# Optimization experiments

Measured on AMD Instinct MI355X. Metric: run time of the kernel, lower is better.

The kernel has to match this reference:

```python
import jax, jax.numpy as jnp
import numpy as np

B, N, K1, M, D = 8, 4096, 17, 2, 256
NT = B * N          # total nodes
EPS = 1e-5          # PyG LayerNorm default eps


def setup_inputs() -> dict:
    key = jax.random.key(0)
    ks = jax.random.split(key, 13)
    s = 1.0 / np.sqrt(D)
    return {
        "x": jax.random.normal(ks[0], (NT, M, D), jnp.float32),
        "knn_edges": jax.random.randint(ks[1], (B, N, K1), 0, N),
        "edge_mask": jax.random.bernoulli(ks[2], 0.9, (B, N, K1)),
        "W0": jax.random.normal(ks[3], (D, D), jnp.float32) * s,
        "b0": jnp.zeros((D,), jnp.float32),
        "g0": jnp.ones((D,), jnp.float32),
        "be0": jnp.zeros((D,), jnp.float32),
        "a0": jnp.full((1,), 0.25, jnp.float32),
        "W1": jax.random.normal(ks[4], (D, D), jnp.float32) * s,
        "b1": jnp.zeros((D,), jnp.float32),
        "g1": jnp.ones((D,), jnp.float32),
        "be1": jnp.zeros((D,), jnp.float32),
        "a1": jnp.full((1,), 0.25, jnp.float32),
    }


def knn_to_edges(knn_edges, edge_mask):
    # drop self column 0, add per-graph batch offsets; keep fixed E with 0/1 weights
    e = knn_edges[:, :, 1:]                       # [B, N, K]
    m = edge_mask[:, :, 1:]
    off = (jnp.arange(B) * N)[:, None, None]      # [B,1,1]
    src = jnp.broadcast_to(jnp.arange(N)[None, :, None] + off, e.shape).reshape(-1)
    dst = (e + off).reshape(-1)
    w = m.reshape(-1).astype(jnp.float32)         # invalid edges -> weight 0
    return src, dst, w


def gcn_conv(h_in, W, b, src, dst, w):
    # PyG GCNConv: add self-loops (weight 1), symmetric normalization
    h = h_in @ W                                            # [NT, D]
    deg = jax.ops.segment_sum(w, dst, num_segments=NT) + 1.0
    dinv = jax.lax.rsqrt(deg)                               # [NT]
    norm = dinv[src] * w * dinv[dst]                        # [E]
    agg = jax.ops.segment_sum(norm[:, None] * h[src], dst, num_segments=NT)
    agg = agg + (dinv * dinv)[:, None] * h                  # self-loop term
    return agg + b


def graph_layernorm(x, g, b):
    # PyG LayerNorm mode='graph', batch=None: normalize over all nodes+features
    xc = x - jnp.mean(x)
    std = jnp.sqrt(jnp.mean(xc * xc))
    return g * (xc / (std + EPS)) + b


def prelu(x, a):
    return jnp.where(x >= 0, x, a * x)


def reference(x, knn_edges, edge_mask, W0, b0, g0, be0, a0, W1, b1, g1, be1, a1):
    src, dst, w = knn_to_edges(knn_edges, edge_mask)
    h = x[:, 0, :]                                          # [NT, D]
    for (W, b, g, be, a) in ((W0, b0, g0, be0, a0), (W1, b1, g1, be1, a1)):
        h = gcn_conv(h, W, b, src, dst, w)
        h = graph_layernorm(h, g, be)
        h = prelu(h, a)
    return h
```

## Files before the change

### kernel.cpp

```cpp
#include <hip/hip_runtime.h>
#include <hip/hip_bf16.h>
#include <stdint.h>

#define B_   8
#define N_   4096
#define K1_  17
#define D_   256
#define NT_  (B_*N_)
#define E16_ (NT_*16)
#define NP_  (NT_*D_)
#define EPS_ 1e-5f

typedef __attribute__((ext_vector_type(8))) short short8v;
typedef __attribute__((ext_vector_type(4))) float f32x4;

__device__ __forceinline__ unsigned short f2bfu(float f){
  unsigned u = __float_as_uint(f);
  unsigned r = (u + 0x7FFFu + ((u>>16)&1u)) >> 16;
  return (unsigned short)r;
}
__device__ __forceinline__ short f2bf(float f){ return (short)f2bfu(f); }
__device__ __forceinline__ unsigned pkbf(float lo, float hi){
  return (unsigned)f2bfu(lo) | ((unsigned)f2bfu(hi) << 16);
}
__device__ __forceinline__ float bf2f(short s){
  return __uint_as_float(((unsigned)(unsigned short)s) << 16);
}
__device__ __forceinline__ void unpack2(unsigned u, float& lo, float& hi){
  lo = __uint_as_float(u << 16);
  hi = __uint_as_float(u & 0xFFFF0000u);
}

__global__ __launch_bounds__(256) void k_prep(const float* __restrict__ W0,
                                              const float* __restrict__ W1,
                                              short* __restrict__ Wt0,
                                              short* __restrict__ Wt1,
                                              int* __restrict__ degcnt,
                                              const unsigned int* __restrict__ mw,
                                              int* __restrict__ flag){
  if (blockIdx.x < 128){
    const float* W  = (blockIdx.x & 1) ? W1  : W0;
    short*       Wt = (blockIdx.x & 1) ? Wt1 : Wt0;
    int tile = blockIdx.x >> 1;
    int ti = tile >> 3, tj = tile & 7;
    __shared__ float sm[32][33];
    int r = threadIdx.x >> 5, c = threadIdx.x & 31;
    #pragma unroll
    for (int i=0;i<4;i++)
      sm[r + i*8][c] = W[(ti*32 + r + i*8)*256 + tj*32 + c];
    __syncthreads();
    #pragma unroll
    for (int i=0;i<4;i++){
      int rr = r + i*8;
      Wt[(size_t)(tj*32 + rr)*256 + ti*32 + c] = f2bf(sm[c][rr]);
    }
  } else {
    int ib = blockIdx.x - 128;
    int i  = ib*256 + threadIdx.x;
    degcnt[i] = 0;
    if (ib == 0){
      __shared__ int s_int, s_f32;
      if (threadIdx.x==0){ s_int=1; s_f32=1; }
      __syncthreads();
      int bad_i=0, bad_f=0;
      #pragma unroll
      for (int j=0;j<4;j++){
        unsigned w = mw[threadIdx.x*4 + j];
        if (!(w==0u || w==1u))          bad_i=1;
        if (!(w==0u || w==0x3F800000u)) bad_f=1;
      }
      if (bad_i) atomicAnd(&s_int, 0);
      if (bad_f) atomicAnd(&s_f32, 0);
      __syncthreads();
      if (threadIdx.x==0) *flag = s_int ? 0 : (s_f32 ? 1 : 2);
    }
  }
}

__device__ __forceinline__ bool mask_at(const void* maskp, int f, int idx){
  if (f==0) return ((const int*)maskp)[idx] != 0;
  if (f==1) return ((const float*)maskp)[idx] != 0.0f;
  return ((const unsigned char*)maskp)[idx] != 0;
}

__global__ void k_deg(const int* __restrict__ knn, const void* __restrict__ maskp,
                      const int* __restrict__ flag, int* __restrict__ degcnt){
  int f = *flag;
  int bid = blockIdx.x;
  int e = ((bid & 7) << 16) + ((bid >> 3) << 8) + threadIdx.x;
  int node = e >> 4;
  int k    = (e & 15) + 1;
  int idx  = node*K1_ + k;
  if (mask_at(maskp, f, idx)){
    int b   = node >> 12;
    int dst = knn[idx] + (b<<12);
    atomicAdd(&degcnt[dst], 1);
  }
}

__global__ void k_scan(const int* __restrict__ degcnt, int* __restrict__ rowptr,
                       int* __restrict__ fillptr, float* __restrict__ dinv){
  __shared__ int wsum[16];
  int t = threadIdx.x;
  int lane = t & 63, wid = t >> 6;
  int base = t*32;
  int loc[32]; int tot = 0;
  #pragma unroll
  for (int i=0;i<32;i++){ loc[i] = degcnt[base+i]; tot += loc[i]; }
  int inc = tot;
  #pragma unroll
  for (int off=1; off<64; off<<=1){
    int v = __shfl_up(inc, off, 64);
    if (lane >= off) inc += v;
  }
  if (lane == 63) wsum[wid] = inc;
  __syncthreads();
  int woff = 0;
  #pragma unroll
  for (int i=0;i<16;i++) if (i < wid) woff += wsum[i];
  int run = woff + inc - tot;
  #pragma unroll
  for (int i=0;i<32;i++){
    int v = base+i;
    rowptr[v]  = run;
    fillptr[v] = run;
    dinv[v]    = rsqrtf((float)loc[i] + 1.0f);
    run += loc[i];
  }
  if (t==1023) rowptr[NT_] = run;
}

__device__ __forceinline__ void g_mfma4(const short* lA, const short* lB,
                                        int wr, int wc, int lr, int qg,
                                        f32x4 (&acc)[4][4]){
  #pragma unroll
  for (int ks=0; ks<2; ks++){
    short8v af[4], bfr[4];
    #pragma unroll
    for (int m=0;m<4;m++){
      int row = wr*64 + m*16 + lr;
      af[m] = *(const short8v*)(lA + (row*8 + ((ks*4+qg) ^ (row&7)))*8);
    }
    #pragma unroll
    for (int n=0;n<4;n++){
      int coln = wc*64 + n*16 + lr;
      bfr[n] = *(const short8v*)(lB + (coln*8 + ((ks*4+qg) ^ (coln&7)))*8);
    }
    #pragma unroll
    for (int m=0;m<4;m++)
      #pragma unroll
      for (int n=0;n<4;n++)
        acc[m][n] = __builtin_amdgcn_mfma_f32_16x16x32_bf16(af[m], bfr[n], acc[m][n], 0, 0, 0);
  }
}

__device__ __forceinline__ void g_cstore(short* __restrict__ C, int rowB,
                                         int wr, int wc, int lr, int qg,
                                         const f32x4 (&acc)[4][4]){
  #pragma unroll
  for (int m=0;m<4;m++){
    int crow = rowB + wr*64 + m*16 + qg*4;
    #pragma unroll
    for (int n=0;n<4;n++){
      int ccol = wc*64 + n*16 + lr;
      #pragma unroll
      for (int r=0;r<4;r++)
        C[(size_t)(crow + r)*256 + ccol] = f2bf(acc[m][n][r]);
    }
  }
}

__global__ __launch_bounds__(512, 4) void k_gemm_x_fill(const float* __restrict__ X,
                                                        const short* __restrict__ Wt,
                                                        short* __restrict__ C,
                                                        const int* __restrict__ knn,
                                                        const void* __restrict__ maskp,
                                                        const int* __restrict__ flag,
                                                        int* __restrict__ fillptr,
                                                        int* __restrict__ col){
  __shared__ short lA[128*64];
  __shared__ short lB[256*64];
  if (blockIdx.x >= 256){
    int f = *flag;
    int fb = (int)blockIdx.x - 256;
    int e  = ((fb & 7) << 16) + ((fb >> 3) << 9) + threadIdx.x;
    int node = e >> 4;
    int k    = (e & 15) + 1;
    int idx  = node*K1_ + k;
    if (mask_at(maskp, f, idx)){
      int b   = node >> 12;
      int dst = knn[idx] + (b<<12);
      int pos = atomicAdd(&fillptr[dst], 1);
      col[pos] = node;
    }
    return;
  }
  int lb   = (int)(blockIdx.x & 7)*32 + (int)(blockIdx.x >> 3);
  int rowB = lb*128;

  int t    = threadIdx.x;
  int wave = t >> 6, lane = t & 63;
  int lr   = lane & 15, qg = lane >> 4;
  int wr   = wave >> 2, wc = wave & 3;

  f32x4 acc[4][4];
  #pragma unroll
  for (int m=0;m<4;m++)
    #pragma unroll
    for (int n=0;n<4;n++) acc[m][n] = (f32x4){0.f,0.f,0.f,0.f};

  int saA[2], scA[2], saB[4], scB[4];
  #pragma unroll
  for (int i=0;i<2;i++){ int e = t + i*512; saA[i] = e>>3; scA[i] = e&7; }
  #pragma unroll
  for (int i=0;i<4;i++){ int e = t + i*512; saB[i] = e>>3; scB[i] = e&7; }

  float4 rax[2], ray[2]; uint4 rb[4];
  #pragma unroll
  for (int i=0;i<2;i++){
    const float* ap = X + (size_t)(rowB+saA[i])*512 + scA[i]*8;
    rax[i] = *(const float4*)ap;
    ray[i] = *(const float4*)(ap+4);
  }
  #pragma unroll
  for (int i=0;i<4;i++)
    rb[i] = *(const uint4*)(Wt + (size_t)saB[i]*256 + scB[i]*8);

  for (int kc=0; kc<4; kc++){
    if (kc) __syncthreads();
    #pragma unroll
    for (int i=0;i<2;i++){
      int ph = saA[i]*8 + (scA[i] ^ (saA[i]&7));
      uint4 cv;
      cv.x = pkbf(rax[i].x, rax[i].y); cv.y = pkbf(rax[i].z, rax[i].w);
      cv.z = pkbf(ray[i].x, ray[i].y); cv.w = pkbf(ray[i].z, ray[i].w);
      *(uint4*)(lA + ph*8) = cv;
    }
    #pragma unroll
    for (int i=0;i<4;i++){
      int ph = saB[i]*8 + (scB[i] ^ (saB[i]&7));
      *(uint4*)(lB + ph*8) = rb[i];
    }
    __syncthreads();
    if (kc < 3){
      #pragma unroll
      for (int i=0;i<2;i++){
        const float* ap = X + (size_t)(rowB+saA[i])*512 + (kc+1)*64 + scA[i]*8;
        rax[i] = *(const float4*)ap;
        ray[i] = *(const float4*)(ap+4);
      }
      #pragma unroll
      for (int i=0;i<4;i++)
        rb[i] = *(const uint4*)(Wt + (size_t)saB[i]*256 + (kc+1)*64 + scB[i]*8);
    }
    g_mfma4(lA, lB, wr, wc, lr, qg, acc);
  }
  g_cstore(C, rowB, wr, wc, lr, qg, acc);
}

__global__ __launch_bounds__(512, 4) void k_gemm_n(const unsigned* __restrict__ BaggU,
                                                   const float* __restrict__ g,
                                                   const float* __restrict__ be,
                                                   const float* __restrict__ aP,
                                                   const float* __restrict__ partS,
                                                   const float* __restrict__ partQ,
                                                   const short* __restrict__ Wt,
                                                   short* __restrict__ C){
  __shared__ short lA[128*64];
  __shared__ short lB[256*64];
  float mean, inv;
  {
    double* sS = (double*)lA;
    double* sQ = (double*)(lA + 4096);
    double a=0.0, b=0.0;
    for (int i=threadIdx.x; i<4096; i+=512){ a += (double)partS[i]; b += (double)partQ[i]; }
    sS[threadIdx.x]=a; sQ[threadIdx.x]=b;
    __syncthreads();
    for (int off=256; off>0; off>>=1){
      if ((int)threadIdx.x < off){ sS[threadIdx.x]+=sS[threadIdx.x+off]; sQ[threadIdx.x]+=sQ[threadIdx.x+off]; }
      __syncthreads();
    }
    if (threadIdx.x==0){
      double m   = sS[0] / (double)NP_;
      double var = sQ[0] / (double)NP_ - m*m;
      var = var > 0.0 ? var : 0.0;
      ((float*)lA)[0] = (float)m;
      ((float*)lA)[1] = (float)(1.0 / (sqrt(var) + (double)EPS_));
    }
    __syncthreads();
    mean = ((float*)lA)[0];
    inv  = ((float*)lA)[1];
    __syncthreads();
  }
  float a = aP[0];

  int lb   = (int)(blockIdx.x & 7)*32 + (int)(blockIdx.x >> 3);
  int rowB = lb*128;

  int t    = threadIdx.x;
  int wave = t >> 6, lane = t & 63;
  int lr   = lane & 15, qg = lane >> 4;
  int wr   = wave >> 2, wc = wave & 3;

  f32x4 acc[4][4];
  #pragma unroll
  for (int m=0;m<4;m++)
    #pragma unroll
    for (int n=0;n<4;n++) acc[m][n] = (f32x4){0.f,0.f,0.f,0.f};

  int saA[2], scA[2], saB[4], scB[4];
  #pragma unroll
  for (int i=0;i<2;i++){ int e = t + i*512; saA[i] = e>>3; scA[i] = e&7; }
  #pragma unroll
  for (int i=0;i<4;i++){ int e = t + i*512; saB[i] = e>>3; scB[i] = e&7; }

  uint4 ra[2], rb[4];
  #pragma unroll
  for (int i=0;i<2;i++)
    ra[i] = *(const uint4*)(BaggU + (size_t)(rowB+saA[i])*128 + scA[i]*4);
  #pragma unroll
  for (int i=0;i<4;i++)
    rb[i] = *(const uint4*)(Wt + (size_t)saB[i]*256 + scB[i]*8);

  for (int kc=0; kc<4; kc++){
    if (kc) __syncthreads();
    #pragma unroll
    for (int i=0;i<2;i++){
      int ph = saA[i]*8 + (scA[i] ^ (saA[i]&7));
      int c0 = kc*64 + scA[i]*8;
      float4 g0 = *(const float4*)&g[c0],  g1 = *(const float4*)&g[c0+4];
      float4 e0 = *(const float4*)&be[c0], e1 = *(const float4*)&be[c0+4];
      float v[8];
      unpack2(ra[i].x, v[0], v[1]); unpack2(ra[i].y, v[2], v[3]);
      unpack2(ra[i].z, v[4], v[5]); unpack2(ra[i].w, v[6], v[7]);
      float gg[8] = {g0.x,g0.y,g0.z,g0.w,g1.x,g1.y,g1.z,g1.w};
      float eb[8] = {e0.x,e0.y,e0.z,e0.w,e1.x,e1.y,e1.z,e1.w};
      float o[8];
      #pragma unroll
      for (int j=0;j<8;j++){
        float tt = gg[j]*((v[j]-mean)*inv) + eb[j];
        o[j] = tt>=0.f ? tt : a*tt;
      }
      uint4 cv;
      cv.x = pkbf(o[0],o[1]); cv.y = pkbf(o[2],o[3]);
      cv.z = pkbf(o[4],o[5]); cv.w = pkbf(o[6],o[7]);
      *(uint4*)(lA + ph*8) = cv;
    }
    #pragma unroll
    for (int i=0;i<4;i++){
      int ph = saB[i]*8 + (scB[i] ^ (saB[i]&7));
      *(uint4*)(lB + ph*8) = rb[i];
    }
    __syncthreads();
    if (kc < 3){
      #pragma unroll
      for (int i=0;i<2;i++)
        ra[i] = *(const uint4*)(BaggU + (size_t)(rowB+saA[i])*128 + (kc+1)*32 + scA[i]*4);
      #pragma unroll
      for (int i=0;i<4;i++)
        rb[i] = *(const uint4*)(Wt + (size_t)saB[i]*256 + (kc+1)*64 + scB[i]*8);
    }
    g_mfma4(lA, lB, wr, wc, lr, qg, acc);
  }
  g_cstore(C, rowB, wr, wc, lr, qg, acc);
}

__global__ __launch_bounds__(256) void k_agg(const short* __restrict__ Ab,
    const int* __restrict__ rowptr, const int* __restrict__ col,
    const float* __restrict__ dinv, const float* __restrict__ bvec,
    unsigned* __restrict__ outU, float* __restrict__ partS, float* __restrict__ partQ){
  int bid  = (int)(blockIdx.x & 7) * 512 + (int)(blockIdx.x >> 3);
  int node = bid*8 + (threadIdx.x >> 5);
  int sub  = threadIdx.x & 31;
  int c0   = sub*8;
  float dv = dinv[node];

  float acc[8];
  {
    short8v s = *(const short8v*)&Ab[(size_t)node*256 + c0];
    #pragma unroll
    for (int i=0;i<8;i++) acc[i] = dv * bf2f(s[i]);
  }
  int j0 = rowptr[node], j1 = rowptr[node+1];
  for (int base=j0; base<j1; base+=32){
    int n = j1 - base; n = n < 32 ? n : 32;
    int   myc = (sub < n) ? col[base+sub] : 0;
    float myd = (sub < n) ? dinv[myc]     : 0.f;
    for (int j=0;j<n;j++){
      int   s  = __shfl(myc, j, 32);
      float ds = __shfl(myd, j, 32);
      short8v nb = *(const short8v*)&Ab[(size_t)s*256 + c0];
      #pragma unroll
      for (int i=0;i<8;i++) acc[i] += ds * bf2f(nb[i]);
    }
  }
  float sum=0.f, sq=0.f;
  float o[8];
  #pragma unroll
  for (int i=0;i<8;i++){
    float v = dv*acc[i] + bvec[c0+i];
    o[i] = v;
    sum += v; sq += v*v;
  }
  uint4 ov;
  ov.x = pkbf(o[0],o[1]); ov.y = pkbf(o[2],o[3]);
  ov.z = pkbf(o[4],o[5]); ov.w = pkbf(o[6],o[7]);
  *(uint4*)&outU[(size_t)node*128 + sub*4] = ov;

  #pragma unroll
  for (int off=16; off>0; off>>=1){
    sum += __shfl_down(sum, off, 32);
    sq  += __shfl_down(sq,  off, 32);
  }
  __shared__ float ls1[8], ls2[8];
  if (sub==0){ ls1[threadIdx.x>>5]=sum; ls2[threadIdx.x>>5]=sq; }
  __syncthreads();
  if (threadIdx.x==0){
    float a=0.f, b=0.f;
    #pragma unroll
    for (int i=0;i<8;i++){ a+=ls1[i]; b+=ls2[i]; }
    partS[bid]=a; partQ[bid]=b;
  }
}

__global__ __launch_bounds__(256) void k_norm_f32(const unsigned* __restrict__ inU,
    const float* __restrict__ g, const float* __restrict__ be,
    const float* __restrict__ aP, const float* __restrict__ partS,
    const float* __restrict__ partQ, float* __restrict__ out){
  __shared__ double sS[256], sQ[256];
  __shared__ float s_mean, s_inv;
  {
    double a=0.0, b=0.0;
    for (int i=threadIdx.x; i<4096; i+=256){ a += (double)partS[i]; b += (double)partQ[i]; }
    sS[threadIdx.x]=a; sQ[threadIdx.x]=b;
    __syncthreads();
    for (int off=128; off>0; off>>=1){
      if ((int)threadIdx.x < off){ sS[threadIdx.x]+=sS[threadIdx.x+off]; sQ[threadIdx.x]+=sQ[threadIdx.x+off]; }
      __syncthreads();
    }
    if (threadIdx.x==0){
      double m   = sS[0] / (double)NP_;
      double var = sQ[0] / (double)NP_ - m*m;
      var = var > 0.0 ? var : 0.0;
      s_mean = (float)m;
      s_inv  = (float)(1.0 / (sqrt(var) + (double)EPS_));
    }
    __syncthreads();
  }
  float mean = s_mean, inv = s_inv, a = aP[0];
  #pragma unroll
  for (int it=0; it<4; it++){
    int gid   = it*(1024*256) + blockIdx.x*256 + threadIdx.x;
    int base8 = gid*8;
    int c0    = base8 & (D_-1);
    uint4 vin = *(const uint4*)&inU[gid*4];
    float4 g0 = *(const float4*)&g[c0],  g1 = *(const float4*)&g[c0+4];
    float4 e0 = *(const float4*)&be[c0], e1 = *(const float4*)&be[c0+4];
    float v[8];
    unpack2(vin.x, v[0], v[1]); unpack2(vin.y, v[2], v[3]);
    unpack2(vin.z, v[4], v[5]); unpack2(vin.w, v[6], v[7]);
    float gg[8] = {g0.x,g0.y,g0.z,g0.w,g1.x,g1.y,g1.z,g1.w};
    float eb[8] = {e0.x,e0.y,e0.z,e0.w,e1.x,e1.y,e1.z,e1.w};
    f32x4 o0, o1;
    #pragma unroll
    for (int i=0;i<8;i++){
      float tt = gg[i]*((v[i]-mean)*inv) + eb[i];
      tt = tt>=0.f ? tt : a*tt;
      if (i<4) o0[i] = tt; else o1[i-4] = tt;
    }
    *(f32x4*)&out[base8]     = o0;
    *(f32x4*)&out[base8 + 4] = o1;
  }
}


extern "C" void kernel_launch(void* const* d_in, const int* in_sizes, int n_in,
                              void* d_out, int out_size, void* d_ws, size_t ws_size,
                              hipStream_t stream){
  const float* x    = (const float*)d_in[0];
  const int*   knn  = (const int*)  d_in[1];
  const void*  mask =               d_in[2];
  const float* W0   = (const float*)d_in[3];
  const float* b0   = (const float*)d_in[4];
  const float* g0   = (const float*)d_in[5];
  const float* be0  = (const float*)d_in[6];
  const float* a0   = (const float*)d_in[7];
  const float* W1   = (const float*)d_in[8];
  const float* b1   = (const float*)d_in[9];
  const float* g1   = (const float*)d_in[10];
  const float* be1  = (const float*)d_in[11];
  const float* a1   = (const float*)d_in[12];
  float* out = (float*)d_out;

  char* w = (char*)d_ws;
  size_t off = 0;
  auto alloc = [&](size_t bytes)->void*{
    void* p = w + off; off = (off + bytes + 255) & ~(size_t)255; return p;
  };
  int*      degcnt  = (int*)     alloc(NT_*4);
  int*      rowptr  = (int*)     alloc((NT_+1)*4);
  int*      fillptr = (int*)     alloc(NT_*4);
  int*      col     = (int*)     alloc(E16_*4);
  float*    dinv    = (float*)   alloc(NT_*4);
  float*    partS   = (float*)   alloc(4096*4);
  float*    partQ   = (float*)   alloc(4096*4);
  int*      flag    = (int*)     alloc(4);
  short*    Ab      = (short*)   alloc((size_t)NP_*2);
  unsigned* Bagg    = (unsigned*)alloc((size_t)NP_*2);
  short*    Wt0     = (short*)   alloc(256*256*2);
  short*    Wt1     = (short*)   alloc(256*256*2);

  hipLaunchKernelGGL(k_prep,  dim3(256),      dim3(256), 0, stream, W0, W1, Wt0, Wt1,
                     degcnt, (const unsigned int*)mask, flag);
  hipLaunchKernelGGL(k_deg,   dim3(E16_/256), dim3(256), 0, stream, knn, mask, flag, degcnt);
  hipLaunchKernelGGL(k_scan,  dim3(1),        dim3(1024),0, stream, degcnt, rowptr, fillptr, dinv);

  hipLaunchKernelGGL(k_gemm_x_fill, dim3(1280), dim3(512), 0, stream, x, Wt0, Ab,
                     knn, mask, flag, fillptr, col);
  hipLaunchKernelGGL(k_agg,    dim3(NT_/8),   dim3(256), 0, stream, Ab, rowptr, col, dinv, b0, Bagg, partS, partQ);

  hipLaunchKernelGGL(k_gemm_n, dim3(256),     dim3(512), 0, stream, Bagg, g0, be0, a0,
                     partS, partQ, Wt1, Ab);
  hipLaunchKernelGGL(k_agg,    dim3(NT_/8),   dim3(256), 0, stream, Ab, rowptr, col, dinv, b1, Bagg, partS, partQ);
  hipLaunchKernelGGL(k_norm_f32, dim3(1024),  dim3(256), 0, stream, Bagg, g1, be1, a1,
                     partS, partQ, out);
}
```

Before: 157.5 us.

## Double-buffer LDS tiles with K=32 chunks in both GEMM kernels

Both GEMM kernels now step through K in 32-wide chunks and alternate between two LDS buffers. The next chunk is written into the other buffer while MFMAs run on the current one, which leaves one barrier per step instead of two. The swizzle pattern moves from 8-way to 4-way, and total LDS per block stays at 48KB. The cost is eight iterations with less MFMA work each, so barrier and loop overhead per step make up a larger share.

```diff
diff --git a/kernel.cpp b/kernel.cpp
--- a/kernel.cpp
+++ b/kernel.cpp
@@ -130,28 +130,25 @@
   if (t==1023) rowptr[NT_] = run;
 }
 
-__device__ __forceinline__ void g_mfma4(const short* lA, const short* lB,
+__device__ __forceinline__ void g_mfma1(const short* cA, const short* cB,
                                         int wr, int wc, int lr, int qg,
                                         f32x4 (&acc)[4][4]){
-  #pragma unroll
-  for (int ks=0; ks<2; ks++){
-    short8v af[4], bfr[4];
-    #pragma unroll
-    for (int m=0;m<4;m++){
-      int row = wr*64 + m*16 + lr;
-      af[m] = *(const short8v*)(lA + (row*8 + ((ks*4+qg) ^ (row&7)))*8);
-    }
-    #pragma unroll
-    for (int n=0;n<4;n++){
-      int coln = wc*64 + n*16 + lr;
-      bfr[n] = *(const short8v*)(lB + (coln*8 + ((ks*4+qg) ^ (coln&7)))*8);
-    }
-    #pragma unroll
-    for (int m=0;m<4;m++)
-      #pragma unroll
-      for (int n=0;n<4;n++)
-        acc[m][n] = __builtin_amdgcn_mfma_f32_16x16x32_bf16(af[m], bfr[n], acc[m][n], 0, 0, 0);
-  }
+  short8v af[4], bfr[4];
+  #pragma unroll
+  for (int m=0;m<4;m++){
+    int row = wr*64 + m*16 + lr;
+    af[m] = *(const short8v*)(cA + (row*4 + (qg ^ (row&3)))*8);
+  }
+  #pragma unroll
+  for (int n=0;n<4;n++){
+    int coln = wc*64 + n*16 + lr;
+    bfr[n] = *(const short8v*)(cB + (coln*4 + (qg ^ (coln&3)))*8);
+  }
+  #pragma unroll
+  for (int m=0;m<4;m++)
+    #pragma unroll
+    for (int n=0;n<4;n++)
+      acc[m][n] = __builtin_amdgcn_mfma_f32_16x16x32_bf16(af[m], bfr[n], acc[m][n], 0, 0, 0);
 }
 
 __device__ __forceinline__ void g_cstore(short* __restrict__ C, int rowB,
@@ -178,8 +175,7 @@
                                                         const int* __restrict__ flag,
                                                         int* __restrict__ fillptr,
                                                         int* __restrict__ col){
-  __shared__ short lA[128*64];
-  __shared__ short lB[256*64];
+  __shared__ short lds[24576];
   if (blockIdx.x >= 256){
     int f = *flag;
     int fb = (int)blockIdx.x - 256;
@@ -195,6 +191,8 @@
     }
     return;
   }
+  short* bufA[2] = { lds,        lds + 4096 };
+  short* bufB[2] = { lds + 8192, lds + 16384 };
   int lb   = (int)(blockIdx.x & 7)*32 + (int)(blockIdx.x >> 3);
   int rowB = lb*128;
 
@@ -209,51 +207,50 @@
     #pragma unroll
     for (int n=0;n<4;n++) acc[m][n] = (f32x4){0.f,0.f,0.f,0.f};
 
-  int saA[2], scA[2], saB[4], scB[4];
-  #pragma unroll
-  for (int i=0;i<2;i++){ int e = t + i*512; saA[i] = e>>3; scA[i] = e&7; }
-  #pragma unroll
-  for (int i=0;i<4;i++){ int e = t + i*512; saB[i] = e>>3; scB[i] = e&7; }
-
-  float4 rax[2], ray[2]; uint4 rb[4];
-  #pragma unroll
-  for (int i=0;i<2;i++){
-    const float* ap = X + (size_t)(rowB+saA[i])*512 + scA[i]*8;
-    rax[i] = *(const float4*)ap;
-    ray[i] = *(const float4*)(ap+4);
-  }
-  #pragma unroll
-  for (int i=0;i<4;i++)
-    rb[i] = *(const uint4*)(Wt + (size_t)saB[i]*256 + scB[i]*8);
-
-  for (int kc=0; kc<4; kc++){
-    if (kc) __syncthreads();
-    #pragma unroll
-    for (int i=0;i<2;i++){
-      int ph = saA[i]*8 + (scA[i] ^ (saA[i]&7));
+  int aRow = t >> 2, aCh = t & 3;
+  int phA  = (aRow*4 + (aCh ^ (aRow&3)))*8;
+  int bRow0 = t >> 2, bRow1 = (t >> 2) + 128, bCh = t & 3;
+  int phB0 = (bRow0*4 + (bCh ^ (bRow0&3)))*8;
+  int phB1 = (bRow1*4 + (bCh ^ (bRow1&3)))*8;
+  const float* aBase  = X  + (size_t)(rowB+aRow)*512 + aCh*8;
+  const short* bBase0 = Wt + (size_t)bRow0*256 + bCh*8;
+  const short* bBase1 = Wt + (size_t)bRow1*256 + bCh*8;
+
+  float4 ra0, ra1; uint4 rb0, rb1;
+  ra0 = *(const float4*)aBase; ra1 = *(const float4*)(aBase+4);
+  rb0 = *(const uint4*)bBase0; rb1 = *(const uint4*)bBase1;
+  {
+    uint4 cv;
+    cv.x = pkbf(ra0.x, ra0.y); cv.y = pkbf(ra0.z, ra0.w);
+    cv.z = pkbf(ra1.x, ra1.y); cv.w = pkbf(ra1.z, ra1.w);
+    *(uint4*)(bufA[0] + phA) = cv;
+    *(uint4*)(bufB[0] + phB0) = rb0;
+    *(uint4*)(bufB[0] + phB1) = rb1;
+  }
+  ra0 = *(const float4*)(aBase + 32); ra1 = *(const float4*)(aBase + 36);
+  rb0 = *(const uint4*)(bBase0 + 32); rb1 = *(const uint4*)(bBase1 + 32);
+  __syncthreads();
+
+  #pragma unroll
+  for (int kc=0; kc<8; kc++){
+    if (kc < 7){
+      short* dA = bufA[(kc+1)&1];
+      short* dB = bufB[(kc+1)&1];
       uint4 cv;
-      cv.x = pkbf(rax[i].x, rax[i].y); cv.y = pkbf(rax[i].z, rax[i].w);
-      cv.z = pkbf(ray[i].x, ray[i].y); cv.w = pkbf(ray[i].z, ray[i].w);
-      *(uint4*)(lA + ph*8) = cv;
-    }
-    #pragma unroll
-    for (int i=0;i<4;i++){
-      int ph = saB[i]*8 + (scB[i] ^ (saB[i]&7));
-      *(uint4*)(lB + ph*8) = rb[i];
-    }
-    __syncthreads();
-    if (kc < 3){
-      #pragma unroll
-      for (int i=0;i<2;i++){
-        const float* ap = X + (size_t)(rowB+saA[i])*512 + (kc+1)*64 + scA[i]*8;
-        rax[i] = *(const float4*)ap;
-        ray[i] = *(const float4*)(ap+4);
-      }
-      #pragma unroll
-      for (int i=0;i<4;i++)
-        rb[i] = *(const uint4*)(Wt + (size_t)saB[i]*256 + (kc+1)*64 + scB[i]*8);
-    }
-    g_mfma4(lA, lB, wr, wc, lr, qg, acc);
+      cv.x = pkbf(ra0.x, ra0.y); cv.y = pkbf(ra0.z, ra0.w);
+      cv.z = pkbf(ra1.x, ra1.y); cv.w = pkbf(ra1.z, ra1.w);
+      *(uint4*)(dA + phA) = cv;
+      *(uint4*)(dB + phB0) = rb0;
+      *(uint4*)(dB + phB1) = rb1;
+    }
+    if (kc < 6){
+      const float* ap = aBase + (kc+2)*32;
+      ra0 = *(const float4*)ap; ra1 = *(const float4*)(ap+4);
+      rb0 = *(const uint4*)(bBase0 + (kc+2)*32);
+      rb1 = *(const uint4*)(bBase1 + (kc+2)*32);
+    }
+    g_mfma1(bufA[kc&1], bufB[kc&1], wr, wc, lr, qg, acc);
+    __syncthreads();
   }
   g_cstore(C, rowB, wr, wc, lr, qg, acc);
 }
@@ -266,12 +263,11 @@
                                                    const float* __restrict__ partQ,
                                                    const short* __restrict__ Wt,
                                                    short* __restrict__ C){
-  __shared__ short lA[128*64];
-  __shared__ short lB[256*64];
+  __shared__ short lds[24576];
   float mean, inv;
   {
-    double* sS = (double*)lA;
-    double* sQ = (double*)(lA + 4096);
+    double* sS = (double*)lds;
+    double* sQ = (double*)(lds + 2048);
     double a=0.0, b=0.0;
     for (int i=threadIdx.x; i<4096; i+=512){ a += (double)partS[i]; b += (double)partQ[i]; }
     sS[threadIdx.x]=a; sQ[threadIdx.x]=b;
@@ -284,16 +280,18 @@
       double m   = sS[0] / (double)NP_;
       double var = sQ[0] / (double)NP_ - m*m;
       var = var > 0.0 ? var : 0.0;
-      ((float*)lA)[0] = (float)m;
-      ((float*)lA)[1] = (float)(1.0 / (sqrt(var) + (double)EPS_));
-    }
-    __syncthreads();
-    mean = ((float*)lA)[0];
-    inv  = ((float*)lA)[1];
+      ((float*)lds)[0] = (float)m;
+      ((float*)lds)[1] = (float)(1.0 / (sqrt(var) + (double)EPS_));
+    }
+    __syncthreads();
+    mean = ((float*)lds)[0];
+    inv  = ((float*)lds)[1];
     __syncthreads();
   }
   float a = aP[0];
 
+  short* bufA[2] = { lds,        lds + 4096 };
+  short* bufB[2] = { lds + 8192, lds + 16384 };
   int lb   = (int)(blockIdx.x & 7)*32 + (int)(blockIdx.x >> 3);
   int rowB = lb*128;
 
@@ -308,59 +306,62 @@
     #pragma unroll
     for (int n=0;n<4;n++) acc[m][n] = (f32x4){0.f,0.f,0.f,0.f};
 
-  int saA[2], scA[2], saB[4], scB[4];
-  #pragma unroll
-  for (int i=0;i<2;i++){ int e = t + i*512; saA[i] = e>>3; scA[i] = e&7; }
-  #pragma unroll
-  for (int i=0;i<4;i++){ int e = t + i*512; saB[i] = e>>3; scB[i] = e&7; }
-
-  uint4 ra[2], rb[4];
-  #pragma unroll
-  for (int i=0;i<2;i++)
-    ra[i] = *(const uint4*)(BaggU + (size_t)(rowB+saA[i])*128 + scA[i]*4);
-  #pragma unroll
-  for (int i=0;i<4;i++)
-    rb[i] = *(const uint4*)(Wt + (size_t)saB[i]*256 + scB[i]*8);
-
-  for (int kc=0; kc<4; kc++){
-    if (kc) __syncthreads();
-    #pragma unroll
-    for (int i=0;i<2;i++){
-      int ph = saA[i]*8 + (scA[i] ^ (saA[i]&7));
-      int c0 = kc*64 + scA[i]*8;
-      float4 g0 = *(const float4*)&g[c0],  g1 = *(const float4*)&g[c0+4];
-      float4 e0 = *(const float4*)&be[c0], e1 = *(const float4*)&be[c0+4];
-      float v[8];
-      unpack2(ra[i].x, v[0], v[1]); unpack2(ra[i].y, v[2], v[3]);
-      unpack2(ra[i].z, v[4], v[5]); unpack2(ra[i].w, v[6], v[7]);
-      float gg[8] = {g0.x,g0.y,g0.z,g0.w,g1.x,g1.y,g1.z,g1.w};
-      float eb[8] = {e0.x,e0.y,e0.z,e0.w,e1.x,e1.y,e1.z,e1.w};
-      float o[8];
-      #pragma unroll
-      for (int j=0;j<8;j++){
-        float tt = gg[j]*((v[j]-mean)*inv) + eb[j];
-        o[j] = tt>=0.f ? tt : a*tt;
-      }
-      uint4 cv;
-      cv.x = pkbf(o[0],o[1]); cv.y = pkbf(o[2],o[3]);
-      cv.z = pkbf(o[4],o[5]); cv.w = pkbf(o[6],o[7]);
-      *(uint4*)(lA + ph*8) = cv;
-    }
-    #pragma unroll
-    for (int i=0;i<4;i++){
-      int ph = saB[i]*8 + (scB[i] ^ (saB[i]&7));
-      *(uint4*)(lB + ph*8) = rb[i];
-    }
-    __syncthreads();
-    if (kc < 3){
-      #pragma unroll
-      for (int i=0;i<2;i++)
-        ra[i] = *(const uint4*)(BaggU + (size_t)(rowB+saA[i])*128 + (kc+1)*32 + scA[i]*4);
-      #pragma unroll
-      for (int i=0;i<4;i++)
-        rb[i] = *(const uint4*)(Wt + (size_t)saB[i]*256 + (kc+1)*64 + scB[i]*8);
-    }
-    g_mfma4(lA, lB, wr, wc, lr, qg, acc);
+  int aRow = t >> 2, aCh = t & 3;
+  int phA  = (aRow*4 + (aCh ^ (aRow&3)))*8;
+  int bRow0 = t >> 2, bRow1 = (t >> 2) + 128, bCh = t & 3;
+  int phB0 = (bRow0*4 + (bCh ^ (bRow0&3)))*8;
+  int phB1 = (bRow1*4 + (bCh ^ (bRow1&3)))*8;
+  const unsigned* aBase = BaggU + (size_t)(rowB+aRow)*128 + aCh*4;
+  const short* bBase0 = Wt + (size_t)bRow0*256 + bCh*8;
+  const short* bBase1 = Wt + (size_t)bRow1*256 + bCh*8;
+
+  auto normWrite = [&](short* dA, uint4 raw, int kc){
+    int c0 = kc*32 + aCh*8;
+    float4 g0 = *(const float4*)&g[c0],  g1 = *(const float4*)&g[c0+4];
+    float4 e0 = *(const float4*)&be[c0], e1 = *(const float4*)&be[c0+4];
+    float v[8];
+    unpack2(raw.x, v[0], v[1]); unpack2(raw.y, v[2], v[3]);
+    unpack2(raw.z, v[4], v[5]); unpack2(raw.w, v[6], v[7]);
+    float gg[8] = {g0.x,g0.y,g0.z,g0.w,g1.x,g1.y,g1.z,g1.w};
+    float eb[8] = {e0.x,e0.y,e0.z,e0.w,e1.x,e1.y,e1.z,e1.w};
+    float o[8];
+    #pragma unroll
+    for (int j=0;j<8;j++){
+      float tt = gg[j]*((v[j]-mean)*inv) + eb[j];
+      o[j] = tt>=0.f ? tt : a*tt;
+    }
+    uint4 cv;
+    cv.x = pkbf(o[0],o[1]); cv.y = pkbf(o[2],o[3]);
+    cv.z = pkbf(o[4],o[5]); cv.w = pkbf(o[6],o[7]);
+    *(uint4*)(dA + phA) = cv;
+  };
+
+  uint4 ra, rb0, rb1;
+  ra  = *(const uint4*)aBase;
+  rb0 = *(const uint4*)bBase0; rb1 = *(const uint4*)bBase1;
+  normWrite(bufA[0], ra, 0);
+  *(uint4*)(bufB[0] + phB0) = rb0;
+  *(uint4*)(bufB[0] + phB1) = rb1;
+  ra  = *(const uint4*)(aBase + 16);
+  rb0 = *(const uint4*)(bBase0 + 32); rb1 = *(const uint4*)(bBase1 + 32);
+  __syncthreads();
+
+  #pragma unroll
+  for (int kc=0; kc<8; kc++){
+    if (kc < 7){
+      short* dA = bufA[(kc+1)&1];
+      short* dB = bufB[(kc+1)&1];
+      normWrite(dA, ra, kc+1);
+      *(uint4*)(dB + phB0) = rb0;
+      *(uint4*)(dB + phB1) = rb1;
+    }
+    if (kc < 6){
+      ra  = *(const uint4*)(aBase + (kc+2)*16);
+      rb0 = *(const uint4*)(bBase0 + (kc+2)*32);
+      rb1 = *(const uint4*)(bBase1 + (kc+2)*32);
+    }
+    g_mfma1(bufA[kc&1], bufB[kc&1], wr, wc, lr, qg, acc);
+    __syncthreads();
   }
   g_cstore(C, rowB, wr, wc, lr, qg, acc);
 }
```

Result: faster. 150.8 us (median of 2 runs) (-4.3%).
